# Performance work log

Hardware: AMD Instinct MI355X
Metric: run time of the kernel (lower is better)

The kernel has to match this reference:

```python
import jax, jax.numpy as jnp
import numpy as np

D = 256  # MCB sketch/output dimension


def count_sketch(x, h, s, d=D):
    # x: [B,H,W,C] channel-last; h: [C] int hash indices in [0,d); s: [C] +/-1 signs
    xs = x * s
    return jnp.zeros(x.shape[:-1] + (d,), x.dtype).at[..., h].add(xs)


def mcb(x, y, h1, s1, h2, s2, d=D):
    # Compact bilinear pooling per spatial location. x,y: [B,C,H,W] -> [B,d,H,W]
    xt = jnp.moveaxis(x, 1, -1)
    yt = jnp.moveaxis(y, 1, -1)
    fx = jnp.fft.rfft(count_sketch(xt, h1, s1, d), axis=-1)
    fy = jnp.fft.rfft(count_sketch(yt, h2, s2, d), axis=-1)
    out = jnp.fft.irfft(fx * fy, n=d, axis=-1)  # circular convolution of the two sketches
    return jnp.moveaxis(out, -1, 1)


def setup_inputs() -> dict:
    key = jax.random.key(0)
    ks = jax.random.split(key, 10)
    B, C, H, W, ATTR = 64, 256, 28, 28, 300
    entity_feature = jax.random.normal(ks[0], (B, C, H, W), jnp.float32)
    attr_one_hot = jax.random.uniform(ks[1], (B, ATTR), jnp.float32)
    W_emb = jax.random.normal(ks[2], (C, ATTR), jnp.float32) * 0.05
    b_emb = jax.random.normal(ks[3], (C,), jnp.float32) * 0.01
    h1 = jax.random.randint(ks[4], (C,), 0, D, jnp.int32)
    h2 = jax.random.randint(ks[5], (C,), 0, D, jnp.int32)
    s1 = jnp.where(jax.random.bernoulli(ks[6], 0.5, (C,)), 1.0, -1.0).astype(jnp.float32)
    s2 = jnp.where(jax.random.bernoulli(ks[7], 0.5, (C,)), 1.0, -1.0).astype(jnp.float32)
    conv1_w = jax.random.normal(ks[8], (32, C), jnp.float32) * 0.05
    conv2_w = jax.random.normal(ks[9], (1, 32), jnp.float32) * 0.05
    return {"entity_feature": entity_feature, "attr_one_hot": attr_one_hot,
            "W_emb": W_emb, "b_emb": b_emb, "h1": h1, "s1": s1, "h2": h2, "s2": s2,
            "conv1_w": conv1_w, "conv2_w": conv2_w}


def reference(entity_feature, attr_one_hot, W_emb, b_emb, h1, s1, h2, s2, conv1_w, conv2_w):
    # textual embedding: Linear(attr_num -> 256)
    emb = attr_one_hot @ W_emb.T + b_emb                      # [B,256]
    attr = jnp.broadcast_to(emb[:, :, None, None], entity_feature.shape)  # expand_as
    mcb_feat = mcb(attr, entity_feature, h1, s1, h2, s2)      # [B,256,H,W]
    hidden = jax.nn.relu(jnp.einsum('bchw,oc->bohw', mcb_feat, conv1_w))  # conv1x1 256->32
    attr_map = jax.nn.sigmoid(jnp.einsum('bchw,oc->bohw', hidden, conv2_w))  # conv1x1 32->1
    attr_feature = attr_map * entity_feature
    return attr_map, attr_feature
```

## Files before the change

### kernel.cpp

```cpp
#include <hip/hip_runtime.h>
#include <math.h>

#define BATCH 64
#define CC    256
#define ATTRN 300
#define DD    256
#define HW    784
#define HW4   196
#define O1    32
#define TF4   49


__global__ __launch_bounds__(512) void k2_fused(
    const float* __restrict__ attr_one_hot,
    const float* __restrict__ W_emb,
    const float* __restrict__ b_emb,
    const int*   __restrict__ h1,
    const float* __restrict__ s1,
    const float* __restrict__ conv1_w,
    float* __restrict__ corrT)
{
    const int b = blockIdx.x, og = blockIdx.y;
    const int tid = threadIdx.x;
    const int t = tid & 255, kh = tid >> 8;
    const int o0 = og * 8;

    __shared__ float s_attr[ATTRN];
    __shared__ float s_sx[DD];
    __shared__ float s_w1[8][DD];
    __shared__ float s_part[8][DD];

    if (kh == 0) {
        s_sx[t] = 0.f;
        if (t < 75) {
            float4 a = *(const float4*)(attr_one_hot + b * ATTRN + 4 * t);
            *(float4*)&s_attr[4 * t] = a;
        }
    } else {
#pragma unroll
        for (int j = 0; j < 8; ++j) s_w1[j][t] = conv1_w[(o0 + j) * CC + t];
    }
    __syncthreads();

    if (kh == 0) {
        float acc = b_emb[t];
        const float* wr = W_emb + (size_t)t * ATTRN;
#pragma unroll 5
        for (int v = 0; v < 75; ++v) {
            float4 w = *(const float4*)(wr + 4 * v);
            float4 a = *(const float4*)(&s_attr[4 * v]);
            acc += w.x * a.x + w.y * a.y + w.z * a.z + w.w * a.w;
        }
        atomicAdd(&s_sx[h1[t]], s1[t] * acc);
    }
    __syncthreads();

    float acc[8] = {0.f,0.f,0.f,0.f,0.f,0.f,0.f,0.f};
    const int kbase = kh << 7;
    for (int k4 = 0; k4 < 32; ++k4) {
        const int k = kbase + 4 * k4;
        float x0 = s_sx[(k     - t) & 255];
        float x1 = s_sx[(k + 1 - t) & 255];
        float x2 = s_sx[(k + 2 - t) & 255];
        float x3 = s_sx[(k + 3 - t) & 255];
#pragma unroll
        for (int oo = 0; oo < 8; ++oo) {
            float4 w = *(const float4*)&s_w1[oo][k];
            acc[oo] += w.x * x0 + w.y * x1 + w.z * x2 + w.w * x3;
        }
    }
    if (kh == 1) {
#pragma unroll
        for (int oo = 0; oo < 8; ++oo) s_part[oo][t] = acc[oo];
    }
    __syncthreads();
    if (kh == 0) {
        float4 r0, r1;
        r0.x = acc[0] + s_part[0][t]; r0.y = acc[1] + s_part[1][t];
        r0.z = acc[2] + s_part[2][t]; r0.w = acc[3] + s_part[3][t];
        r1.x = acc[4] + s_part[4][t]; r1.y = acc[5] + s_part[5][t];
        r1.z = acc[6] + s_part[6][t]; r1.w = acc[7] + s_part[7][t];
        float4* dst = (float4*)(corrT + ((size_t)b * DD + t) * O1 + o0);
        dst[0] = r0; dst[1] = r1;
    }
}

#define FMA4(A, S, E) { (A).x += (S)*(E).x; (A).y += (S)*(E).y; (A).z += (S)*(E).z; (A).w += (S)*(E).w; }

#define FMA_OCT(BUF, CIDX) { \
    const int c_ = (CIDX); \
    float4 pa = *(const float4*)&sm.Pl[c_][8 * oi]; \
    float4 pb = *(const float4*)&sm.Pl[c_][8 * oi + 4]; \
    FMA4(acc[0], pa.x, BUF); FMA4(acc[1], pa.y, BUF); \
    FMA4(acc[2], pa.z, BUF); FMA4(acc[3], pa.w, BUF); \
    FMA4(acc[4], pb.x, BUF); FMA4(acc[5], pb.y, BUF); \
    FMA4(acc[6], pb.z, BUF); FMA4(acc[7], pb.w, BUF); }

__global__ __launch_bounds__(1024, 4) void k3_main(
    const float* __restrict__ ent,
    const float* __restrict__ corrT,
    const int*   __restrict__ h2,
    const float* __restrict__ s2,
    const float* __restrict__ conv2_w,
    float* __restrict__ out_map,
    float* __restrict__ out_feat)
{
    const int b = blockIdx.x, tile = blockIdx.y;
    const int tid  = threadIdx.x;
    const int wv   = tid >> 6, lane = tid & 63;
    const int ci   = wv >> 2;
    const int oi   = wv & 3;

    union SMem {
        float  Pl[CC][36];
        float4 red[4][TF4][9];
    };
    __shared__ SMem sm;
    __shared__ float4 s_amap4[TF4];
    __shared__ float  s_c2[O1];

    {
        const int c = tid >> 2, qp = tid & 3;
        const int hc = h2[c];
        const float sc = s2[c];
        const float4* src = (const float4*)(corrT + ((size_t)b * DD + hc) * O1);
        float4 x0 = src[2 * qp], x1 = src[2 * qp + 1];
        x0.x *= sc; x0.y *= sc; x0.z *= sc; x0.w *= sc;
        x1.x *= sc; x1.y *= sc; x1.z *= sc; x1.w *= sc;
        *(float4*)&sm.Pl[c][8 * qp]     = x0;
        *(float4*)&sm.Pl[c][8 * qp + 4] = x1;
        if (tid < O1) s_c2[tid] = conv2_w[tid];
    }
    __syncthreads();

    const bool act = lane < TF4;
    const int f4i = tile * TF4 + (act ? lane : TF4 - 1);
    const float4* ent4 = (const float4*)ent;
    const int c0 = ci * 64;

    float4 acc[8];
#pragma unroll
    for (int o = 0; o < 8; ++o) acc[o] = make_float4(0.f, 0.f, 0.f, 0.f);

    const float4* eptr = ent4 + (size_t)(b * CC + c0) * HW4 + f4i;

    float4 bufA[8], bufB[8];
#pragma unroll
    for (int u = 0; u < 8; ++u) bufA[u] = eptr[(size_t)u * HW4];

    for (int cc0 = 0; cc0 < 64; cc0 += 16) {
#pragma unroll
        for (int u = 0; u < 8; ++u) bufB[u] = eptr[(size_t)(cc0 + 8 + u) * HW4];
#pragma unroll
        for (int u = 0; u < 8; ++u) FMA_OCT(bufA[u], c0 + cc0 + u);
#pragma unroll
        for (int u = 0; u < 8; ++u) {
            int idx = cc0 + 16 + u;
            idx = idx > 63 ? 63 : idx;
            bufA[u] = eptr[(size_t)idx * HW4];
        }
#pragma unroll
        for (int u = 0; u < 8; ++u) FMA_OCT(bufB[u], c0 + cc0 + 8 + u);
    }

    float pre = 0.f;
#pragma unroll
    for (int g = 0; g < 4; ++g) {
        __syncthreads();
        if (oi == g && act) {
#pragma unroll
            for (int i = 0; i < 8; ++i) sm.red[ci][lane][i] = acc[i];
        }
        __syncthreads();
        if (tid < 4 * TF4) {
            const int fi = tid >> 2, j = tid & 3;
#pragma unroll
            for (int i = 0; i < 8; ++i) {
                float v = ((const float*)&sm.red[0][fi][i])[j]
                        + ((const float*)&sm.red[1][fi][i])[j]
                        + ((const float*)&sm.red[2][fi][i])[j]
                        + ((const float*)&sm.red[3][fi][i])[j];
                pre += s_c2[8 * g + i] * fmaxf(v, 0.f);
            }
        }
    }
    __syncthreads();
    if (tid < 4 * TF4) {
        const int fi = tid >> 2, j = tid & 3;
        float am = 1.f / (1.f + expf(-pre));
        ((float*)&s_amap4[fi])[j] = am;
        out_map[b * HW + tile * (4 * TF4) + tid] = am;
    }
    __syncthreads();

    const float4 am4 = s_amap4[act ? lane : 0];
    float4* of4 = (float4*)out_feat;
    const int cb = wv * 16;
#pragma unroll 4
    for (int cc = 0; cc < 16; ++cc) {
        const int c = cb + cc;
        if (act) {
            const size_t idx = (size_t)(b * CC + c) * HW4 + f4i;
            float4 e4 = ent4[idx];
            float4 r;
            r.x = am4.x * e4.x; r.y = am4.y * e4.y;
            r.z = am4.z * e4.z; r.w = am4.w * e4.w;
            of4[idx] = r;
        }
    }
}

extern "C" void kernel_launch(void* const* d_in, const int* in_sizes, int n_in,
                              void* d_out, int out_size, void* d_ws, size_t ws_size,
                              hipStream_t stream) {
    const float* ent   = (const float*)d_in[0];
    const float* attr  = (const float*)d_in[1];
    const float* W_emb = (const float*)d_in[2];
    const float* b_emb = (const float*)d_in[3];
    const int*   h1    = (const int*)d_in[4];
    const float* s1    = (const float*)d_in[5];
    const int*   h2    = (const int*)d_in[6];
    const float* s2    = (const float*)d_in[7];
    const float* c1w   = (const float*)d_in[8];
    const float* c2w   = (const float*)d_in[9];

    float* ws    = (float*)d_ws;
    float* corrT = ws + 16384;

    float* out      = (float*)d_out;
    float* out_map  = out;
    float* out_feat = out + BATCH * HW;

    hipLaunchKernelGGL(k2_fused, dim3(BATCH, 4), dim3(512), 0, stream,
                       attr, W_emb, b_emb, h1, s1, c1w, corrT);
    hipLaunchKernelGGL(k3_main, dim3(BATCH, 4), dim3(1024), 0, stream,
                       ent, corrT, h2, s2, c2w, out_map, out_feat);
}
```

Before: 173.9 us.

## Repartition k3 work to 2 channel halves x 8 output quads per wave

Changes the wave decomposition in the main kernel from 4 channel quarters x 4 output octets to 2 channel halves x 8 output quads. Each wave now keeps 4 float4 accumulators and 4-deep load buffers instead of 8, which lowers register pressure and may help occupancy under the 1024-thread launch bound. The cost is that each wave streams twice as many entity channels, so total global reads of the entity tensor double, and the pipelined loads are shallower. The reduction is reindexed to match the new slot layout.

```diff
diff --git a/kernel.cpp b/kernel.cpp
--- a/kernel.cpp
+++ b/kernel.cpp
@@ -87,15 +87,6 @@
 
 #define FMA4(A, S, E) { (A).x += (S)*(E).x; (A).y += (S)*(E).y; (A).z += (S)*(E).z; (A).w += (S)*(E).w; }
 
-#define FMA_OCT(BUF, CIDX) { \
-    const int c_ = (CIDX); \
-    float4 pa = *(const float4*)&sm.Pl[c_][8 * oi]; \
-    float4 pb = *(const float4*)&sm.Pl[c_][8 * oi + 4]; \
-    FMA4(acc[0], pa.x, BUF); FMA4(acc[1], pa.y, BUF); \
-    FMA4(acc[2], pa.z, BUF); FMA4(acc[3], pa.w, BUF); \
-    FMA4(acc[4], pb.x, BUF); FMA4(acc[5], pb.y, BUF); \
-    FMA4(acc[6], pb.z, BUF); FMA4(acc[7], pb.w, BUF); }
-
 __global__ __launch_bounds__(1024, 4) void k3_main(
     const float* __restrict__ ent,
     const float* __restrict__ corrT,
@@ -108,8 +99,8 @@
     const int b = blockIdx.x, tile = blockIdx.y;
     const int tid  = threadIdx.x;
     const int wv   = tid >> 6, lane = tid & 63;
-    const int ci   = wv >> 2;
-    const int oi   = wv & 3;
+    const int ch   = wv >> 3;
+    const int oq   = wv & 7;
 
     union SMem {
         float  Pl[CC][36];
@@ -136,51 +127,63 @@
     const bool act = lane < TF4;
     const int f4i = tile * TF4 + (act ? lane : TF4 - 1);
     const float4* ent4 = (const float4*)ent;
-    const int c0 = ci * 64;
-
-    float4 acc[8];
-#pragma unroll
-    for (int o = 0; o < 8; ++o) acc[o] = make_float4(0.f, 0.f, 0.f, 0.f);
+    const int c0 = ch * 128;
+
+    float4 acc[4];
+#pragma unroll
+    for (int o = 0; o < 4; ++o) acc[o] = make_float4(0.f, 0.f, 0.f, 0.f);
 
     const float4* eptr = ent4 + (size_t)(b * CC + c0) * HW4 + f4i;
 
-    float4 bufA[8], bufB[8];
-#pragma unroll
-    for (int u = 0; u < 8; ++u) bufA[u] = eptr[(size_t)u * HW4];
-
-    for (int cc0 = 0; cc0 < 64; cc0 += 16) {
-#pragma unroll
-        for (int u = 0; u < 8; ++u) bufB[u] = eptr[(size_t)(cc0 + 8 + u) * HW4];
-#pragma unroll
-        for (int u = 0; u < 8; ++u) FMA_OCT(bufA[u], c0 + cc0 + u);
-#pragma unroll
-        for (int u = 0; u < 8; ++u) {
-            int idx = cc0 + 16 + u;
-            idx = idx > 63 ? 63 : idx;
+    float4 bufA[4], bufB[4];
+#pragma unroll
+    for (int u = 0; u < 4; ++u) bufA[u] = eptr[(size_t)u * HW4];
+
+    for (int cc0 = 0; cc0 < 128; cc0 += 8) {
+#pragma unroll
+        for (int u = 0; u < 4; ++u) bufB[u] = eptr[(size_t)(cc0 + 4 + u) * HW4];
+#pragma unroll
+        for (int u = 0; u < 4; ++u) {
+            const int c = c0 + cc0 + u;
+            float4 p = *(const float4*)&sm.Pl[c][4 * oq];
+            FMA4(acc[0], p.x, bufA[u]); FMA4(acc[1], p.y, bufA[u]);
+            FMA4(acc[2], p.z, bufA[u]); FMA4(acc[3], p.w, bufA[u]);
+        }
+#pragma unroll
+        for (int u = 0; u < 4; ++u) {
+            int idx = cc0 + 8 + u;
+            idx = idx > 127 ? 127 : idx;
             bufA[u] = eptr[(size_t)idx * HW4];
         }
 #pragma unroll
-        for (int u = 0; u < 8; ++u) FMA_OCT(bufB[u], c0 + cc0 + 8 + u);
+        for (int u = 0; u < 4; ++u) {
+            const int c = c0 + cc0 + 4 + u;
+            float4 p = *(const float4*)&sm.Pl[c][4 * oq];
+            FMA4(acc[0], p.x, bufB[u]); FMA4(acc[1], p.y, bufB[u]);
+            FMA4(acc[2], p.z, bufB[u]); FMA4(acc[3], p.w, bufB[u]);
+        }
     }
 
     float pre = 0.f;
 #pragma unroll
     for (int g = 0; g < 4; ++g) {
         __syncthreads();
-        if (oi == g && act) {
-#pragma unroll
-            for (int i = 0; i < 8; ++i) sm.red[ci][lane][i] = acc[i];
+        if ((oq >> 1) == g && act) {
+            const int slot = 2 * (oq & 1) + ch;
+#pragma unroll
+            for (int i = 0; i < 4; ++i) sm.red[slot][lane][i] = acc[i];
         }
         __syncthreads();
         if (tid < 4 * TF4) {
             const int fi = tid >> 2, j = tid & 3;
 #pragma unroll
-            for (int i = 0; i < 8; ++i) {
-                float v = ((const float*)&sm.red[0][fi][i])[j]
-                        + ((const float*)&sm.red[1][fi][i])[j]
-                        + ((const float*)&sm.red[2][fi][i])[j]
-                        + ((const float*)&sm.red[3][fi][i])[j];
-                pre += s_c2[8 * g + i] * fmaxf(v, 0.f);
+            for (int i = 0; i < 4; ++i) {
+                float v0 = ((const float*)&sm.red[0][fi][i])[j]
+                         + ((const float*)&sm.red[1][fi][i])[j];
+                float v1 = ((const float*)&sm.red[2][fi][i])[j]
+                         + ((const float*)&sm.red[3][fi][i])[j];
+                pre += s_c2[8 * g + i]     * fmaxf(v0, 0.f);
+                pre += s_c2[8 * g + 4 + i] * fmaxf(v1, 0.f);
             }
         }
     }
```

After: 174.2 us. No clear change (+0.2%).
